# Kernel optimization log

Hardware: AMD Instinct MI355X
Metric: run time of the kernel (lower is better)

The kernel has to match this reference:

```python
import jax, jax.numpy as jnp
import numpy as np

N, IN_C, OUT_C, FEAT_C, G = 1_000_000, 64, 64, 128, 4096


def setup_inputs() -> dict:
    key = jax.random.key(0)
    ks = jax.random.split(key, 9)
    x = jax.random.normal(ks[0], (N, IN_C), dtype=jnp.float32)
    origin_feat = jax.random.normal(ks[1], (G, FEAT_C), dtype=jnp.float32)
    latent_point_batch = jax.random.randint(ks[2], (N,), 0, G, dtype=jnp.int32)
    s_fc = 1.0 / np.sqrt(IN_C)
    s_ft = 1.0 / np.sqrt(FEAT_C)
    W_fc = jax.random.uniform(ks[3], (IN_C, OUT_C), jnp.float32, -s_fc, s_fc)
    b_fc = jax.random.uniform(ks[4], (OUT_C,), jnp.float32, -s_fc, s_fc)
    W_mu = jax.random.uniform(ks[5], (FEAT_C, OUT_C), jnp.float32, -s_ft, s_ft)
    b_mu = jax.random.uniform(ks[6], (OUT_C,), jnp.float32, -s_ft, s_ft)
    W_sig = jax.random.uniform(ks[7], (FEAT_C, OUT_C), jnp.float32, -s_ft, s_ft)
    b_sig = jax.random.uniform(ks[8], (OUT_C,), jnp.float32, -s_ft, s_ft)
    return {"x": x, "origin_feat": origin_feat, "latent_point_batch": latent_point_batch,
            "num_groups": G, "W_fc": W_fc, "b_fc": b_fc, "W_mu": W_mu, "b_mu": b_mu,
            "W_sig": W_sig, "b_sig": b_sig}


def _segment_mean(v, seg, num_segments):
    # [N, C] -> [G, C] per-segment mean
    s = jax.ops.segment_sum(v, seg, num_segments=num_segments)
    cnt = jax.ops.segment_sum(jnp.ones((v.shape[0],), v.dtype), seg,
                              num_segments=num_segments)
    return s / jnp.maximum(cnt, 1.0)[:, None]


def reference(x, origin_feat, latent_point_batch, num_groups,
              W_fc, b_fc, W_mu, b_mu, W_sig, b_sig):
    h = x @ W_fc + b_fc                      # [N, outC]
    mu = origin_feat @ W_mu + b_mu           # [G, outC]
    sig = origin_feat @ W_sig + b_sig        # [G, outC]
    seg = latent_point_batch
    h_mean = _segment_mean(h, seg, num_groups)          # [G, outC]
    h_c = h - h_mean[seg]                                # centered
    h_var = _segment_mean(h_c * h_c, seg, num_groups)    # biased var per group
    h_n = h_c / jnp.sqrt(h_var[seg] + 1e-14)
    out = jax.nn.relu(h_n * sig[seg] + mu[seg])
    return out
```

## Files before the change

### kernel.cpp

```cpp
#include <hip/hip_runtime.h>
#include <hip/hip_bf16.h>
#include <stdint.h>

typedef unsigned int u32;

__global__ void FCAdaINLayer_68719477052_kernel(int* __restrict__ cnt, int G) {
  int t = blockIdx.x * blockDim.x + threadIdx.x;
  int stride = gridDim.x * blockDim.x;
  for (int i = t; i < G; i += stride) cnt[i] = 0;
}

__global__ void k_hist(const int* __restrict__ lat, int n, int* __restrict__ cnt) {
  int i = blockIdx.x * blockDim.x + threadIdx.x;
  int stride = gridDim.x * blockDim.x;
  for (; i < n; i += stride) atomicAdd(&cnt[lat[i]], 1);
}

__global__ void k_scan(const int* __restrict__ cnt, int G, int* __restrict__ offs,
                       int* __restrict__ cursor) {
  __shared__ int part[256];
  int t = threadIdx.x;
  int per = (G + 255) / 256;
  int base = t * per;
  int s = 0;
  for (int j = 0; j < per; j++) { int g = base + j; if (g < G) s += cnt[g]; }
  part[t] = s;
  __syncthreads();
  if (t == 0) {
    int run = 0;
    for (int j = 0; j < 256; j++) { int v = part[j]; part[j] = run; run += v; }
  }
  __syncthreads();
  int run = part[t];
  for (int j = 0; j < per; j++) {
    int g = base + j;
    if (g < G) { offs[g] = run; cursor[g] = run; run += cnt[g]; }
  }
  if (t == 255) offs[G] = run;
}

__global__ void k_scatter(const int* __restrict__ lat, int n, int* __restrict__ cursor,
                          int* __restrict__ sorted) {
  int i = blockIdx.x * blockDim.x + threadIdx.x;
  int stride = gridDim.x * blockDim.x;
  for (; i < n; i += stride) {
    int g = lat[i];
    int pos = atomicAdd(&cursor[g], 1);
    sorted[pos] = i;
  }
}

__global__ void k_musig(const float* __restrict__ of, const float* __restrict__ Wmu,
                        const float* __restrict__ bmu, const float* __restrict__ Wsig,
                        const float* __restrict__ bsig, float* __restrict__ mug,
                        float* __restrict__ sgg, int total) {
  int idx = blockIdx.x * blockDim.x + threadIdx.x;
  if (idx >= total) return;
  int g = idx >> 6, c = idx & 63;
  const float* ofr = of + (size_t)g * 128;
  float a0 = 0.f, a1 = 0.f;
  for (int k = 0; k < 128; k++) {
    float ov = ofr[k];
    a0 = fmaf(ov, Wmu[k * 64 + c], a0);
    a1 = fmaf(ov, Wsig[k * 64 + c], a1);
  }
  mug[idx] = a0 + bmu[c];
  sgg[idx] = a1 + bsig[c];
}

__device__ __forceinline__ float dot64(const float4* __restrict__ xr,
                                       const float* wcol, float bc) {
  float h0 = bc, h1 = 0.f, h2 = 0.f, h3 = 0.f;
#pragma unroll
  for (int j = 0; j < 16; j++) {
    float4 q = xr[j];
    int k = j * 4;
    h0 = fmaf(q.x, wcol[k], h0);
    h1 = fmaf(q.y, wcol[k + 1], h1);
    h2 = fmaf(q.z, wcol[k + 2], h2);
    h3 = fmaf(q.w, wcol[k + 3], h3);
  }
  return (h0 + h2) + (h1 + h3);
}

#define ROWS 312
__global__ __launch_bounds__(256) void k_main(
    const float* __restrict__ x, const int* __restrict__ sorted,
    const int* __restrict__ offs, const float* __restrict__ mug,
    const float* __restrict__ sgg, const float* __restrict__ Wfc,
    const float* __restrict__ bfc, float* __restrict__ out) {
  __shared__ float xs[ROWS * 64];
  __shared__ float red[2][4][64];
  int g = blockIdx.x;
  int beg = offs[g], end = offs[g + 1];
  int cnt = end - beg;
  if (cnt == 0) return;
  int tid = threadIdx.x;
  int lane = tid & 63, wid = tid >> 6;
  int rows = cnt < ROWS ? cnt : ROWS;

  for (int idx = tid; idx < rows * 16; idx += 256) {
    int j = idx >> 4, e = idx & 15;
    int p = sorted[beg + j];
    reinterpret_cast<float4*>(xs)[j * 16 + e] =
        reinterpret_cast<const float4*>(x + (size_t)p * 64)[e];
  }
  __syncthreads();

  float wcol[64];
#pragma unroll
  for (int k = 0; k < 64; k++) wcol[k] = Wfc[k * 64 + lane];
  float bc = bfc[lane];

  float ssum = 0.f, ssq = 0.f;
  for (int j = wid; j < cnt; j += 8) {
    int j2 = j + 4;
    float h1;
    if (j < ROWS) {
      h1 = dot64(reinterpret_cast<const float4*>(xs + j * 64), wcol, bc);
      xs[j * 64 + lane] = h1;
    } else {
      int p = __builtin_amdgcn_readfirstlane(sorted[beg + j]);
      h1 = dot64(reinterpret_cast<const float4*>(x + (size_t)p * 64), wcol, bc);
    }
    ssum += h1;
    ssq = fmaf(h1, h1, ssq);
    if (j2 < cnt) {
      float h2;
      if (j2 < ROWS) {
        h2 = dot64(reinterpret_cast<const float4*>(xs + j2 * 64), wcol, bc);
        xs[j2 * 64 + lane] = h2;
      } else {
        int p = __builtin_amdgcn_readfirstlane(sorted[beg + j2]);
        h2 = dot64(reinterpret_cast<const float4*>(x + (size_t)p * 64), wcol, bc);
      }
      ssum += h2;
      ssq = fmaf(h2, h2, ssq);
    }
  }
  red[0][wid][lane] = ssum;
  red[1][wid][lane] = ssq;
  __syncthreads();
  float ts = 0.f, tq = 0.f;
#pragma unroll
  for (int w = 0; w < 4; w++) { ts += red[0][w][lane]; tq += red[1][w][lane]; }
  float inv = 1.0f / (float)cnt;
  float mean = ts * inv;
  float var = fmaxf(tq * inv - mean * mean, 0.f);
  float rstd = rsqrtf(var + 1e-14f);
  float scale = sgg[(size_t)g * 64 + lane] * rstd;
  float shift = mug[(size_t)g * 64 + lane] - mean * scale;

  for (int j = wid; j < cnt; j += 4) {
    int p = __builtin_amdgcn_readfirstlane(sorted[beg + j]);
    float h;
    if (j < ROWS) {
      h = xs[j * 64 + lane];
    } else {
      h = dot64(reinterpret_cast<const float4*>(x + (size_t)p * 64), wcol, bc);
    }
    out[(size_t)p * 64 + lane] = fmaxf(fmaf(h, scale, shift), 0.f);
  }
}

extern "C" void kernel_launch(void* const* d_in, const int* in_sizes, int n_in,
                              void* d_out, int out_size, void* d_ws, size_t ws_size,
                              hipStream_t stream) {
  const float* x   = (const float*)d_in[0];
  const float* of  = (const float*)d_in[1];
  const int* lat   = (const int*)d_in[2];
  const float* Wfc = (const float*)d_in[4];
  const float* bfc = (const float*)d_in[5];
  const float* Wmu = (const float*)d_in[6];
  const float* bmu = (const float*)d_in[7];
  const float* Wsg = (const float*)d_in[8];
  const float* bsg = (const float*)d_in[9];

  int N = in_sizes[2];
  int G = in_sizes[1] / 128;

  char* ws = (char*)d_ws;
  size_t o = 0;
  int* cnt    = (int*)(ws + o); o += (size_t)G * 4;
  int* offs   = (int*)(ws + o); o += (size_t)(G + 1) * 4;
  int* cursor = (int*)(ws + o); o += (size_t)G * 4;
  o = (o + 255) & ~(size_t)255;
  float* mug  = (float*)(ws + o); o += (size_t)G * 64 * 4;
  float* sgg  = (float*)(ws + o); o += (size_t)G * 64 * 4;
  int* sorted = (int*)(ws + o); o += (size_t)N * 4;

  FCAdaINLayer_68719477052_kernel<<<32, 256, 0, stream>>>(cnt, G);
  k_hist<<<1024, 256, 0, stream>>>(lat, N, cnt);
  k_scan<<<1, 256, 0, stream>>>(cnt, G, offs, cursor);
  k_scatter<<<1024, 256, 0, stream>>>(lat, N, cursor, sorted);
  k_musig<<<(G * 64 + 255) / 256, 256, 0, stream>>>(of, Wmu, bmu, Wsg, bsg, mug, sgg, G * 64);
  k_main<<<G, 256, 0, stream>>>(x, sorted, offs, mug, sgg, Wfc, bfc, (float*)d_out);
}
```

Before: 958.3 us.

## Split into stats and streaming apply passes with block-local histogram sort

Replaces global-atomic histogram and scatter with per-block shared-memory histograms, a column scan and block-local cursors, which makes the sorted index order deterministic and cuts global atomic contention. The fused per-group kernel becomes a stats-only pass that processes gathered rows in 64-row chunks and also computes mu/sigma, writing per-group scale and shift. A new streaming kernel then reads x in its original order, recomputes the FC output and applies the affine plus ReLU with coalesced writes. The cost is reading x twice and computing the 64x64 matmul twice, in exchange for coalesced output writes and no large per-group shared-memory cache.

```diff
diff --git a/kernel.cpp b/kernel.cpp
--- a/kernel.cpp
+++ b/kernel.cpp
@@ -1,8 +1,9 @@
 #include <hip/hip_runtime.h>
-#include <hip/hip_bf16.h>
 #include <stdint.h>
 
-typedef unsigned int u32;
+#define GMAX 4096
+#define NB   256
+#define CH   64
 
 __global__ void FCAdaINLayer_68719477052_kernel(int* __restrict__ cnt, int G) {
   int t = blockIdx.x * blockDim.x + threadIdx.x;
@@ -10,14 +11,32 @@
   for (int i = t; i < G; i += stride) cnt[i] = 0;
 }
 
-__global__ void k_hist(const int* __restrict__ lat, int n, int* __restrict__ cnt) {
-  int i = blockIdx.x * blockDim.x + threadIdx.x;
-  int stride = gridDim.x * blockDim.x;
-  for (; i < n; i += stride) atomicAdd(&cnt[lat[i]], 1);
-}
-
-__global__ void k_scan(const int* __restrict__ cnt, int G, int* __restrict__ offs,
-                       int* __restrict__ cursor) {
+__global__ __launch_bounds__(256) void k_bhist(const int* __restrict__ lat, int n, int G,
+                                               int* __restrict__ hist_b) {
+  __shared__ int h[GMAX];
+  int b = blockIdx.x, t = threadIdx.x;
+  for (int g = t; g < G; g += 256) h[g] = 0;
+  __syncthreads();
+  int chb = (n + NB - 1) / NB;
+  int beg = b * chb, end = min(beg + chb, n);
+  for (int i = beg + t; i < end; i += 256) atomicAdd(&h[lat[i]], 1);
+  __syncthreads();
+  for (int g = t; g < G; g += 256) hist_b[(size_t)b * G + g] = h[g];
+}
+
+__global__ void k_scanA(int* __restrict__ hist_b, int G, int* __restrict__ cnt) {
+  int g = blockIdx.x * blockDim.x + threadIdx.x;
+  if (g >= G) return;
+  int run = 0;
+  for (int b = 0; b < NB; b++) {
+    int v = hist_b[(size_t)b * G + g];
+    hist_b[(size_t)b * G + g] = run;
+    run += v;
+  }
+  cnt[g] = run;
+}
+
+__global__ void k_scanB(const int* __restrict__ cnt, int G, int* __restrict__ offs) {
   __shared__ int part[256];
   int t = threadIdx.x;
   int per = (G + 255) / 256;
@@ -34,38 +53,26 @@
   int run = part[t];
   for (int j = 0; j < per; j++) {
     int g = base + j;
-    if (g < G) { offs[g] = run; cursor[g] = run; run += cnt[g]; }
+    if (g < G) { offs[g] = run; run += cnt[g]; }
   }
   if (t == 255) offs[G] = run;
 }
 
-__global__ void k_scatter(const int* __restrict__ lat, int n, int* __restrict__ cursor,
-                          int* __restrict__ sorted) {
-  int i = blockIdx.x * blockDim.x + threadIdx.x;
-  int stride = gridDim.x * blockDim.x;
-  for (; i < n; i += stride) {
+__global__ __launch_bounds__(256) void k_scatter2(const int* __restrict__ lat, int n, int G,
+                                                  const int* __restrict__ offs,
+                                                  const int* __restrict__ hist_b,
+                                                  int* __restrict__ sorted) {
+  __shared__ int cur[GMAX];
+  int b = blockIdx.x, t = threadIdx.x;
+  for (int g = t; g < G; g += 256) cur[g] = offs[g] + hist_b[(size_t)b * G + g];
+  __syncthreads();
+  int chb = (n + NB - 1) / NB;
+  int beg = b * chb, end = min(beg + chb, n);
+  for (int i = beg + t; i < end; i += 256) {
     int g = lat[i];
-    int pos = atomicAdd(&cursor[g], 1);
+    int pos = atomicAdd(&cur[g], 1);
     sorted[pos] = i;
   }
-}
-
-__global__ void k_musig(const float* __restrict__ of, const float* __restrict__ Wmu,
-                        const float* __restrict__ bmu, const float* __restrict__ Wsig,
-                        const float* __restrict__ bsig, float* __restrict__ mug,
-                        float* __restrict__ sgg, int total) {
-  int idx = blockIdx.x * blockDim.x + threadIdx.x;
-  if (idx >= total) return;
-  int g = idx >> 6, c = idx & 63;
-  const float* ofr = of + (size_t)g * 128;
-  float a0 = 0.f, a1 = 0.f;
-  for (int k = 0; k < 128; k++) {
-    float ov = ofr[k];
-    a0 = fmaf(ov, Wmu[k * 64 + c], a0);
-    a1 = fmaf(ov, Wsig[k * 64 + c], a1);
-  }
-  mug[idx] = a0 + bmu[c];
-  sgg[idx] = a1 + bsig[c];
 }
 
 __device__ __forceinline__ float dot64(const float4* __restrict__ xr,
@@ -83,29 +90,20 @@
   return (h0 + h2) + (h1 + h3);
 }
 
-#define ROWS 312
-__global__ __launch_bounds__(256) void k_main(
+__global__ __launch_bounds__(256) void k_stats(
     const float* __restrict__ x, const int* __restrict__ sorted,
-    const int* __restrict__ offs, const float* __restrict__ mug,
-    const float* __restrict__ sgg, const float* __restrict__ Wfc,
-    const float* __restrict__ bfc, float* __restrict__ out) {
-  __shared__ float xs[ROWS * 64];
+    const int* __restrict__ offs, const float* __restrict__ of,
+    const float* __restrict__ Wmu, const float* __restrict__ bmu,
+    const float* __restrict__ Wsig, const float* __restrict__ bsig,
+    const float* __restrict__ Wfc, const float* __restrict__ bfc,
+    float* __restrict__ scaleT, float* __restrict__ shiftT) {
+  __shared__ float xs[CH * 64];
   __shared__ float red[2][4][64];
   int g = blockIdx.x;
   int beg = offs[g], end = offs[g + 1];
   int cnt = end - beg;
   if (cnt == 0) return;
-  int tid = threadIdx.x;
-  int lane = tid & 63, wid = tid >> 6;
-  int rows = cnt < ROWS ? cnt : ROWS;
-
-  for (int idx = tid; idx < rows * 16; idx += 256) {
-    int j = idx >> 4, e = idx & 15;
-    int p = sorted[beg + j];
-    reinterpret_cast<float4*>(xs)[j * 16 + e] =
-        reinterpret_cast<const float4*>(x + (size_t)p * 64)[e];
-  }
-  __syncthreads();
+  int tid = threadIdx.x, lane = tid & 63, wid = tid >> 6;
 
   float wcol[64];
 #pragma unroll
@@ -113,53 +111,78 @@
   float bc = bfc[lane];
 
   float ssum = 0.f, ssq = 0.f;
-  for (int j = wid; j < cnt; j += 8) {
-    int j2 = j + 4;
-    float h1;
-    if (j < ROWS) {
-      h1 = dot64(reinterpret_cast<const float4*>(xs + j * 64), wcol, bc);
-      xs[j * 64 + lane] = h1;
-    } else {
-      int p = __builtin_amdgcn_readfirstlane(sorted[beg + j]);
-      h1 = dot64(reinterpret_cast<const float4*>(x + (size_t)p * 64), wcol, bc);
-    }
-    ssum += h1;
-    ssq = fmaf(h1, h1, ssq);
-    if (j2 < cnt) {
-      float h2;
-      if (j2 < ROWS) {
-        h2 = dot64(reinterpret_cast<const float4*>(xs + j2 * 64), wcol, bc);
-        xs[j2 * 64 + lane] = h2;
-      } else {
-        int p = __builtin_amdgcn_readfirstlane(sorted[beg + j2]);
-        h2 = dot64(reinterpret_cast<const float4*>(x + (size_t)p * 64), wcol, bc);
-      }
-      ssum += h2;
-      ssq = fmaf(h2, h2, ssq);
+  for (int c0 = 0; c0 < cnt; c0 += CH) {
+    int rows = min(CH, cnt - c0);
+    __syncthreads();
+    for (int idx = tid; idx < rows * 16; idx += 256) {
+      int j = idx >> 4, e = idx & 15;
+      int p = sorted[beg + c0 + j];
+      reinterpret_cast<float4*>(xs)[j * 16 + e] =
+          reinterpret_cast<const float4*>(x + (size_t)p * 64)[e];
+    }
+    __syncthreads();
+    for (int j = wid; j < rows; j += 4) {
+      float h = dot64(reinterpret_cast<const float4*>(xs + j * 64), wcol, bc);
+      ssum += h;
+      ssq = fmaf(h, h, ssq);
     }
   }
   red[0][wid][lane] = ssum;
   red[1][wid][lane] = ssq;
   __syncthreads();
-  float ts = 0.f, tq = 0.f;
-#pragma unroll
-  for (int w = 0; w < 4; w++) { ts += red[0][w][lane]; tq += red[1][w][lane]; }
-  float inv = 1.0f / (float)cnt;
-  float mean = ts * inv;
-  float var = fmaxf(tq * inv - mean * mean, 0.f);
-  float rstd = rsqrtf(var + 1e-14f);
-  float scale = sgg[(size_t)g * 64 + lane] * rstd;
-  float shift = mug[(size_t)g * 64 + lane] - mean * scale;
-
-  for (int j = wid; j < cnt; j += 4) {
-    int p = __builtin_amdgcn_readfirstlane(sorted[beg + j]);
-    float h;
-    if (j < ROWS) {
-      h = xs[j * 64 + lane];
-    } else {
-      h = dot64(reinterpret_cast<const float4*>(x + (size_t)p * 64), wcol, bc);
-    }
-    out[(size_t)p * 64 + lane] = fmaxf(fmaf(h, scale, shift), 0.f);
+  if (wid == 0) {
+    float ts = 0.f, tq = 0.f;
+#pragma unroll
+    for (int w = 0; w < 4; w++) { ts += red[0][w][lane]; tq += red[1][w][lane]; }
+    float inv = 1.0f / (float)cnt;
+    float mean = ts * inv;
+    float var = fmaxf(tq * inv - mean * mean, 0.f);
+    float rstd = rsqrtf(var + 1e-14f);
+    const float* ofr = of + (size_t)g * 128;
+    float a0 = 0.f, a1 = 0.f;
+    for (int k = 0; k < 128; k++) {
+      float ov = ofr[k];
+      a0 = fmaf(ov, Wmu[k * 64 + lane], a0);
+      a1 = fmaf(ov, Wsig[k * 64 + lane], a1);
+    }
+    float mu = a0 + bmu[lane];
+    float sig = a1 + bsig[lane];
+    float sc = sig * rstd;
+    scaleT[(size_t)g * 64 + lane] = sc;
+    shiftT[(size_t)g * 64 + lane] = mu - mean * sc;
+  }
+}
+
+__global__ __launch_bounds__(256) void k_applyn(
+    const float* __restrict__ x, const int* __restrict__ lat, int n,
+    const float* __restrict__ scaleT, const float* __restrict__ shiftT,
+    const float* __restrict__ Wfc, const float* __restrict__ bfc,
+    float* __restrict__ out) {
+  __shared__ float xs[CH * 64];
+  int tid = threadIdx.x, lane = tid & 63, wid = tid >> 6;
+  float wcol[64];
+#pragma unroll
+  for (int k = 0; k < 64; k++) wcol[k] = Wfc[k * 64 + lane];
+  float bc = bfc[lane];
+
+  int nchunks = (n + CH - 1) / CH;
+  for (int c = blockIdx.x; c < nchunks; c += gridDim.x) {
+    int p0 = c * CH;
+    int rows = min(CH, n - p0);
+    __syncthreads();
+    for (int idx = tid; idx < rows * 16; idx += 256) {
+      reinterpret_cast<float4*>(xs)[idx] =
+          reinterpret_cast<const float4*>(x + (size_t)p0 * 64)[idx];
+    }
+    __syncthreads();
+    for (int j = wid; j < rows; j += 4) {
+      int p = p0 + j;
+      int g = lat[p];
+      float h = dot64(reinterpret_cast<const float4*>(xs + j * 64), wcol, bc);
+      float sc = scaleT[(size_t)g * 64 + lane];
+      float sh = shiftT[(size_t)g * 64 + lane];
+      out[(size_t)p * 64 + lane] = fmaxf(fmaf(h, sc, sh), 0.f);
+    }
   }
 }
 
@@ -181,18 +204,19 @@
 
   char* ws = (char*)d_ws;
   size_t o = 0;
-  int* cnt    = (int*)(ws + o); o += (size_t)G * 4;
-  int* offs   = (int*)(ws + o); o += (size_t)(G + 1) * 4;
-  int* cursor = (int*)(ws + o); o += (size_t)G * 4;
+  int* cnt     = (int*)(ws + o); o += (size_t)G * 4;
+  int* offs    = (int*)(ws + o); o += (size_t)(G + 1) * 4;
   o = (o + 255) & ~(size_t)255;
-  float* mug  = (float*)(ws + o); o += (size_t)G * 64 * 4;
-  float* sgg  = (float*)(ws + o); o += (size_t)G * 64 * 4;
-  int* sorted = (int*)(ws + o); o += (size_t)N * 4;
+  int* hist_b  = (int*)(ws + o); o += (size_t)NB * G * 4;
+  int* sorted  = (int*)(ws + o); o += (size_t)N * 4;
+  float* scT   = (float*)(ws + o); o += (size_t)G * 64 * 4;
+  float* shT   = (float*)(ws + o); o += (size_t)G * 64 * 4;
 
   FCAdaINLayer_68719477052_kernel<<<32, 256, 0, stream>>>(cnt, G);
-  k_hist<<<1024, 256, 0, stream>>>(lat, N, cnt);
-  k_scan<<<1, 256, 0, stream>>>(cnt, G, offs, cursor);
-  k_scatter<<<1024, 256, 0, stream>>>(lat, N, cursor, sorted);
-  k_musig<<<(G * 64 + 255) / 256, 256, 0, stream>>>(of, Wmu, bmu, Wsg, bsg, mug, sgg, G * 64);
-  k_main<<<G, 256, 0, stream>>>(x, sorted, offs, mug, sgg, Wfc, bfc, (float*)d_out);
-}
+  k_bhist<<<NB, 256, 0, stream>>>(lat, N, G, hist_b);
+  k_scanA<<<(G + 255) / 256, 256, 0, stream>>>(hist_b, G, cnt);
+  k_scanB<<<1, 256, 0, stream>>>(cnt, G, offs);
+  k_scatter2<<<NB, 256, 0, stream>>>(lat, N, G, offs, hist_b, sorted);
+  k_stats<<<G, 256, 0, stream>>>(x, sorted, offs, of, Wmu, bmu, Wsg, bsg, Wfc, bfc, scT, shT);
+  k_applyn<<<2048, 256, 0, stream>>>(x, lat, N, scT, shT, Wfc, bfc, (float*)d_out);
+}
```

Result: faster. 925.1 us (-3.5%).
